# Optimization experiments

Hardware: AMD Instinct MI355X
Metric: run time of the kernel (lower is better)

The kernel has to match this reference:

```python
import jax, jax.numpy as jnp
import numpy as np

N_NODES = 100000

def gcn_conv(x, W, b, src, dst, n):
    # PyG GCNConv: add self-loops, symmetric normalization, scatter-add aggregation.
    xw = x @ W  # [N, out]
    loop = jnp.arange(n, dtype=src.dtype)
    s = jnp.concatenate([src, loop])
    d = jnp.concatenate([dst, loop])
    deg = jax.ops.segment_sum(jnp.ones_like(d, dtype=xw.dtype), d, num_segments=n)
    inv_sqrt = jnp.where(deg > 0, jax.lax.rsqrt(jnp.maximum(deg, 1.0)), 0.0)
    norm = inv_sqrt[s] * inv_sqrt[d]  # [E+N]
    msg = xw[s] * norm[:, None]       # gather + scale
    out = jax.ops.segment_sum(msg, d, num_segments=n)  # scatter-add
    return out + b

def setup_inputs() -> dict:
    key = jax.random.key(0)
    k = jax.random.split(key, 6)
    x = jax.random.normal(k[0], (N_NODES, 128), dtype=jnp.float32)
    edge_index = jax.random.randint(k[1], (2, 3200000), 0, N_NODES, dtype=jnp.int64 if jax.config.jax_enable_x64 else jnp.int32)
    edge_label_index = jax.random.randint(k[2], (2, 200000), 0, N_NODES, dtype=edge_index.dtype)
    W1 = jax.random.normal(k[3], (128, 32), dtype=jnp.float32) * (1.0 / np.sqrt(128))
    b1 = jnp.zeros((32,), dtype=jnp.float32)
    W2 = jax.random.normal(k[4], (32, 16), dtype=jnp.float32) * (1.0 / np.sqrt(32))
    b2 = jnp.zeros((16,), dtype=jnp.float32)
    return {"x": x, "edge_index": edge_index, "edge_label_index": edge_label_index,
            "W1": W1, "b1": b1, "W2": W2, "b2": b2}

def reference(x, edge_index, edge_label_index, W1, b1, W2, b2):
    src, dst = edge_index[0], edge_index[1]
    n = x.shape[0]
    # encode (eval mode: dropout is identity)
    h = gcn_conv(x, W1, b1, src, dst, n)
    h = jax.nn.relu(h)
    z = gcn_conv(h, W2, b2, src, dst, n)
    # decode: dot product over candidate edges
    logits = jnp.sum(z[edge_label_index[0]] * z[edge_label_index[1]], axis=-1)
    return logits
```

## Files before the change

### kernel.cpp

```cpp
#include <hip/hip_runtime.h>
#include <hip/hip_fp16.h>


#define NPB 512
#define NBMAX 256
#define A3_CHUNK 4096

__global__ __launch_bounds__(256) void k_a1(const int* __restrict__ dst,
                                            int* __restrict__ bcnt, int E, int NB) {
    __shared__ int lb[NBMAX];
    int t = threadIdx.x;
    for (int i = t; i < NB; i += 256) lb[i] = 0;
    __syncthreads();
    for (int e = blockIdx.x * 256 + t; e < E; e += gridDim.x * 256)
        atomicAdd(&lb[dst[e] >> 9], 1);
    __syncthreads();
    for (int i = t; i < NB; i += 256) {
        int c = lb[i];
        if (c) atomicAdd(&bcnt[i], c);
    }
}

__global__ __launch_bounds__(256) void k_scanb(const int* __restrict__ bcnt,
                                               int* __restrict__ bbase,
                                               int* __restrict__ bcursor,
                                               int* __restrict__ pbase, int NB) {
    __shared__ int sh[256];
    int t = threadIdx.x;
    int i0 = t * 4;
    int v[4], p[4];
#pragma unroll
    for (int j = 0; j < 4; ++j) {
        v[j] = (i0 + j < NB) ? bcnt[i0 + j] : 0;
        p[j] = ((v[j] + 3) & ~3) + 3 * NPB;
    }
    sh[t] = v[0] + v[1] + v[2] + v[3];
    __syncthreads();
    for (int off = 1; off < 256; off <<= 1) {
        int add = (t >= off) ? sh[t - off] : 0;
        __syncthreads();
        sh[t] += add;
        __syncthreads();
    }
    int run = (t > 0) ? sh[t - 1] : 0;
    int total = sh[255];
#pragma unroll
    for (int j = 0; j < 4; ++j) {
        if (i0 + j < NB) { bbase[i0 + j] = run; bcursor[i0 + j] = run; }
        run += v[j];
    }
    if (t == 255) bbase[NB] = total;
    __syncthreads();
    sh[t] = p[0] + p[1] + p[2] + p[3];
    __syncthreads();
    for (int off = 1; off < 256; off <<= 1) {
        int add = (t >= off) ? sh[t - off] : 0;
        __syncthreads();
        sh[t] += add;
        __syncthreads();
    }
    int run2 = (t > 0) ? sh[t - 1] : 0;
#pragma unroll
    for (int j = 0; j < 4; ++j) {
        if (i0 + j < NB) pbase[i0 + j] = run2;
        run2 += p[j];
    }
}

__global__ __launch_bounds__(256) void k_a3(const int* __restrict__ src,
                                            const int* __restrict__ dst,
                                            int* __restrict__ bcursor,
                                            unsigned* __restrict__ eb, int E, int NB) {
    __shared__ int lhist[NBMAX];
    __shared__ int lbase[NBMAX];
    int t = threadIdx.x;
    int e0 = blockIdx.x * A3_CHUNK;
    int e1 = min(e0 + A3_CHUNK, E);
    for (int i = t; i < NB; i += 256) lhist[i] = 0;
    __syncthreads();
    for (int e = e0 + t; e < e1; e += 256)
        atomicAdd(&lhist[dst[e] >> 9], 1);
    __syncthreads();
    for (int i = t; i < NB; i += 256) {
        int c = lhist[i];
        lbase[i] = c ? atomicAdd(&bcursor[i], c) : 0;
        lhist[i] = 0;
    }
    __syncthreads();
    for (int e = e0 + t; e < e1; e += 256) {
        int s = src[e], d = dst[e];
        int b = d >> 9;
        int r = atomicAdd(&lhist[b], 1);
        eb[lbase[b] + r] = ((unsigned)s << 9) | (unsigned)(d & 511);
    }
}

__global__ __launch_bounds__(256) void k_csr(const int* __restrict__ bbase,
                                             const int* __restrict__ pbase,
                                             const unsigned* __restrict__ eb,
                                             int* __restrict__ col,
                                             int* __restrict__ rpbeg,
                                             int* __restrict__ rpcnt,
                                             float* __restrict__ inv,
                                             int n, int NB) {
    __shared__ int cnt[4][NPB];
    __shared__ int cur[4][NPB];
    __shared__ int sh[256];
    int t = threadIdx.x, b = blockIdx.x;
    int wv = t >> 6;
    int nbase = b * NPB;
    int beg = bbase[b], end = bbase[b + 1];
    int pb = pbase[b];
    for (int i = t; i < 4 * NPB; i += 256) ((int*)cnt)[i] = 0;
    __syncthreads();
    for (int i = beg + t; i < end; i += 256) atomicAdd(&cnt[wv][eb[i] & 511u], 1);
    __syncthreads();
    int l0 = 2 * t, l1 = 2 * t + 1;
    int c0 = cnt[0][l0] + cnt[1][l0] + cnt[2][l0] + cnt[3][l0];
    int c1 = cnt[0][l1] + cnt[1][l1] + cnt[2][l1] + cnt[3][l1];
    int pc0 = (c0 + 3) & ~3, pc1 = (c1 + 3) & ~3;
    sh[t] = pc0 + pc1;
    __syncthreads();
    for (int off = 1; off < 256; off <<= 1) {
        int v = (t >= off) ? sh[t - off] : 0;
        __syncthreads();
        sh[t] += v;
        __syncthreads();
    }
    int base0 = pb + sh[t] - (pc0 + pc1);
    int base1 = base0 + pc0;
    int run = base0;
#pragma unroll
    for (int r = 0; r < 4; ++r) { cur[r][l0] = run; run += cnt[r][l0]; }
    run = base1;
#pragma unroll
    for (int r = 0; r < 4; ++r) { cur[r][l1] = run; run += cnt[r][l1]; }
    int node0 = nbase + l0, node1 = nbase + l1;
    if (node0 < n) {
        rpbeg[node0] = base0;
        rpcnt[node0] = pc0;
        inv[node0] = rsqrtf((float)(c0 + 1));
        for (int j = c0; j < pc0; ++j) col[base0 + j] = n;
    }
    if (node1 < n) {
        rpbeg[node1] = base1;
        rpcnt[node1] = pc1;
        inv[node1] = rsqrtf((float)(c1 + 1));
        for (int j = c1; j < pc1; ++j) col[base1 + j] = n;
    }
    __syncthreads();
    for (int i = beg + t; i < end; i += 256) {
        unsigned p = eb[i];
        int pos = atomicAdd(&cur[wv][p & 511u], 1);
        col[pos] = (int)(p >> 9);
    }
}

__global__ __launch_bounds__(256) void k_xw(const float* __restrict__ x,
                                            const float* __restrict__ W1,
                                            const float* __restrict__ inv,
                                            uint2* __restrict__ X,
                                            unsigned* __restrict__ hws0, int n) {
    __shared__ float xsh[128 * 128];
    __shared__ float W1s[128 * 32];
    int t = threadIdx.x;
    int base = blockIdx.x * 128;
#pragma unroll
    for (int i = 0; i < 16; ++i) W1s[i * 256 + t] = W1[i * 256 + t];
    {
        int nl = t >> 1, kh = (t & 1) * 64;
        int node = base + nl;
        if (node < n) {
            const float4* xr = (const float4*)(x + (size_t)node * 128 + kh);
#pragma unroll
            for (int kk = 0; kk < 16; ++kk) {
                float4 v = xr[kk];
                int k = kh + kk * 4;
                xsh[(k + 0) * 128 + nl] = v.x;
                xsh[(k + 1) * 128 + nl] = v.y;
                xsh[(k + 2) * 128 + nl] = v.z;
                xsh[(k + 3) * 128 + nl] = v.w;
            }
        } else {
#pragma unroll
            for (int kk = 0; kk < 64; ++kk) xsh[(kh + kk) * 128 + nl] = 0.0f;
        }
    }
    if (blockIdx.x == 0) {
        if (t < 8) X[(size_t)n * 8 + t] = make_uint2(0u, 0u);
        else if (t < 16) hws0[(size_t)n * 8 + (t - 8)] = 0u;
    }
    __syncthreads();
    int tc = t & 7, tr = t >> 3;
    float acc[4][4] = {};
#pragma unroll 8
    for (int k = 0; k < 128; ++k) {
        float4 xv = *(const float4*)&xsh[k * 128 + 4 * tr];
        float4 wv = *(const float4*)&W1s[k * 32 + 4 * tc];
        acc[0][0] += xv.x * wv.x; acc[0][1] += xv.x * wv.y; acc[0][2] += xv.x * wv.z; acc[0][3] += xv.x * wv.w;
        acc[1][0] += xv.y * wv.x; acc[1][1] += xv.y * wv.y; acc[1][2] += xv.y * wv.z; acc[1][3] += xv.y * wv.w;
        acc[2][0] += xv.z * wv.x; acc[2][1] += xv.z * wv.y; acc[2][2] += xv.z * wv.z; acc[2][3] += xv.z * wv.w;
        acc[3][0] += xv.w * wv.x; acc[3][1] += xv.w * wv.y; acc[3][2] += xv.w * wv.z; acc[3][3] += xv.w * wv.w;
    }
#pragma unroll
    for (int i = 0; i < 4; ++i) {
        int node = base + 4 * tr + i;
        if (node < n) {
            float iw = inv[node];
            __half2 p0 = __floats2half2_rn(acc[i][0] * iw, acc[i][1] * iw);
            __half2 p1 = __floats2half2_rn(acc[i][2] * iw, acc[i][3] * iw);
            uint2 u;
            u.x = *(unsigned*)&p0;
            u.y = *(unsigned*)&p1;
            X[(size_t)node * 8 + tc] = u;
        }
    }
}

__device__ __forceinline__ void add4h(float* a, uint2 v) {
    union { uint2 u; __half h[4]; } cv;
    cv.u = v;
#pragma unroll
    for (int j = 0; j < 4; ++j) a[j] = fmaf(__half2float(cv.h[j]), 1.0f, a[j]);
}

__device__ __forceinline__ void add2h(float* a, unsigned v) {
    union { unsigned u; __half h[2]; } cv;
    cv.u = v;
    a[0] = fmaf(__half2float(cv.h[0]), 1.0f, a[0]);
    a[1] = fmaf(__half2float(cv.h[1]), 1.0f, a[1]);
}

__global__ __launch_bounds__(256) void k_agg1(const int* __restrict__ rpbeg,
                                              const int* __restrict__ rpcnt,
                                              const int* __restrict__ col,
                                              const uint2* __restrict__ X2,
                                              const float* __restrict__ inv,
                                              const float* __restrict__ b1,
                                              const float* __restrict__ W2,
                                              __half2* __restrict__ hws, int n) {
    __shared__ float W2s[512];
    int t = threadIdx.x;
    W2s[t] = W2[t];
    W2s[256 + t] = W2[256 + t];
    __syncthreads();
    int w = (blockIdx.x * 256 + t) >> 3;
    if (w >= n) return;
    int q = t & 7;
    int grpbase = (t & 63) & 56;
    float bb[4];
#pragma unroll
    for (int j = 0; j < 4; ++j) bb[j] = b1[4 * q + j];
    int beg = rpbeg[w], endp = beg + rpcnt[w];
    float a[4] = {};
    add4h(a, X2[(size_t)w * 8 + q]);
    for (int i = beg; i < endp; i += 4) {
        int4 c4 = *(const int4*)(col + i);
        uint2 v0 = X2[(size_t)c4.x * 8 + q];
        uint2 v1 = X2[(size_t)c4.y * 8 + q];
        uint2 v2 = X2[(size_t)c4.z * 8 + q];
        uint2 v3 = X2[(size_t)c4.w * 8 + q];
        add4h(a, v0);
        add4h(a, v1);
        add4h(a, v2);
        add4h(a, v3);
    }
    float iw = inv[w];
    float h[4];
#pragma unroll
    for (int j = 0; j < 4; ++j) h[j] = fmaxf(iw * a[j] + bb[j], 0.0f);
    float s0 = 0.0f, s1 = 0.0f;
#pragma unroll
    for (int qq = 0; qq < 8; ++qq) {
#pragma unroll
        for (int j = 0; j < 4; ++j) {
            float hv = __shfl(h[j], grpbase + qq);
            float2 wv = *(const float2*)&W2s[(4 * qq + j) * 16 + 2 * q];
            s0 = fmaf(hv, wv.x, s0);
            s1 = fmaf(hv, wv.y, s1);
        }
    }
    hws[(size_t)w * 8 + q] = __floats2half2_rn(s0 * iw, s1 * iw);
}

__global__ __launch_bounds__(256) void k_agg2(const int* __restrict__ rpbeg,
                                              const int* __restrict__ rpcnt,
                                              const int* __restrict__ col,
                                              const unsigned* __restrict__ H,
                                              const float* __restrict__ inv,
                                              const float* __restrict__ b2,
                                              unsigned* __restrict__ z, int n) {
    int t = threadIdx.x;
    int w = (blockIdx.x * 256 + t) >> 3;
    if (w >= n) return;
    int q = t & 7;
    float bb0 = b2[2 * q], bb1 = b2[2 * q + 1];
    int beg = rpbeg[w], endp = beg + rpcnt[w];
    float a[2] = {};
    add2h(a, H[(size_t)w * 8 + q]);
    for (int i = beg; i < endp; i += 4) {
        int4 c4 = *(const int4*)(col + i);
        unsigned v0 = H[(size_t)c4.x * 8 + q];
        unsigned v1 = H[(size_t)c4.y * 8 + q];
        unsigned v2 = H[(size_t)c4.z * 8 + q];
        unsigned v3 = H[(size_t)c4.w * 8 + q];
        add2h(a, v0);
        add2h(a, v1);
        add2h(a, v2);
        add2h(a, v3);
    }
    float iw = inv[w];
    __half2 r = __floats2half2_rn(iw * a[0] + bb0, iw * a[1] + bb1);
    z[(size_t)w * 8 + q] = *(unsigned*)&r;
}

__device__ __forceinline__ float dot8h(uint4 u, uint4 v, float s) {
    const __half2* pu = (const __half2*)&u;
    const __half2* pv = (const __half2*)&v;
#pragma unroll
    for (int i = 0; i < 4; ++i) {
#if __has_builtin(__builtin_amdgcn_fdot2)
        s = __builtin_amdgcn_fdot2(pu[i], pv[i], s, false);
#else
        float2 a = __half22float2(pu[i]);
        float2 b = __half22float2(pv[i]);
        s += a.x * b.x + a.y * b.y;
#endif
    }
    return s;
}

__global__ void k_decode(const int* __restrict__ eli, const uint4* __restrict__ z4,
                         float* __restrict__ out, int L) {
    int e = blockIdx.x * blockDim.x + threadIdx.x;
    if (e >= L) return;
    int a = eli[e], b = eli[L + e];
    uint4 ua0 = z4[(size_t)a * 2], ua1 = z4[(size_t)a * 2 + 1];
    uint4 ub0 = z4[(size_t)b * 2], ub1 = z4[(size_t)b * 2 + 1];
    out[e] = dot8h(ua1, ub1, dot8h(ua0, ub0, 0.0f));
}

extern "C" void kernel_launch(void* const* d_in, const int* in_sizes, int n_in,
                              void* d_out, int out_size, void* d_ws, size_t ws_size,
                              hipStream_t stream) {
    const float* x   = (const float*)d_in[0];
    const int*   ei  = (const int*)d_in[1];
    const int*   eli = (const int*)d_in[2];
    const float* W1  = (const float*)d_in[3];
    const float* b1  = (const float*)d_in[4];
    const float* W2  = (const float*)d_in[5];
    const float* b2  = (const float*)d_in[6];
    float* out = (float*)d_out;

    int n = in_sizes[0] / 128;
    int E = in_sizes[1] / 2;
    int L = in_sizes[2] / 2;
    const int* src = ei;
    const int* dst = ei + E;
    int NB = (n + NPB - 1) / NPB;

    uint2* X       = (uint2*)d_ws;
    unsigned* hws  = (unsigned*)(X + (size_t)(n + 1) * 8);
    unsigned* z    = hws + (size_t)(n + 1) * 8;
    float* inv     = (float*)(z + (size_t)n * 8);
    int* rpbeg     = (int*)(inv + n);
    int* rpcnt     = rpbeg + n;
    unsigned* eb   = (unsigned*)(rpcnt + n);
    int* col       = (int*)(eb + E);
    int* bcnt      = col + E + 1600 * NB;
    int* bbase     = bcnt + NB;
    int* pbase     = bbase + NB + 1;
    int* bcursor   = pbase + NB + 1;

    hipMemsetAsync(bcnt, 0, NB * sizeof(int), stream);
    k_a1<<<512, 256, 0, stream>>>(dst, bcnt, E, NB);
    k_scanb<<<1, 256, 0, stream>>>(bcnt, bbase, bcursor, pbase, NB);
    k_a3<<<(E + A3_CHUNK - 1) / A3_CHUNK, 256, 0, stream>>>(src, dst, bcursor, eb, E, NB);
    k_csr<<<NB, 256, 0, stream>>>(bbase, pbase, eb, col, rpbeg, rpcnt, inv, n, NB);
    k_xw<<<(n + 127) / 128, 256, 0, stream>>>(x, W1, inv, X, hws, n);
    k_agg1<<<((size_t)n * 8 + 255) / 256, 256, 0, stream>>>(rpbeg, rpcnt, col, X, inv, b1, W2, (__half2*)hws, n);
    k_agg2<<<((size_t)n * 8 + 255) / 256, 256, 0, stream>>>(rpbeg, rpcnt, col, hws, inv, b2, z, n);
    k_decode<<<(L + 255) / 256, 256, 0, stream>>>(eli, (const uint4*)z, out, L);
}
```

Baseline: 313.4 us.

## Replace atomic bucket partition with deterministic per-chunk histogram, scan and LDS-staged scatter

```diff
diff --git a/kernel.cpp b/kernel.cpp
--- a/kernel.cpp
+++ b/kernel.cpp
@@ -4,99 +4,99 @@
 
 #define NPB 512
 #define NBMAX 256
-#define A3_CHUNK 4096
-
-__global__ __launch_bounds__(256) void k_a1(const int* __restrict__ dst,
-                                            int* __restrict__ bcnt, int E, int NB) {
-    __shared__ int lb[NBMAX];
-    int t = threadIdx.x;
-    for (int i = t; i < NB; i += 256) lb[i] = 0;
-    __syncthreads();
-    for (int e = blockIdx.x * 256 + t; e < E; e += gridDim.x * 256)
-        atomicAdd(&lb[dst[e] >> 9], 1);
-    __syncthreads();
-    for (int i = t; i < NB; i += 256) {
-        int c = lb[i];
-        if (c) atomicAdd(&bcnt[i], c);
-    }
-}
-
-__global__ __launch_bounds__(256) void k_scanb(const int* __restrict__ bcnt,
-                                               int* __restrict__ bbase,
-                                               int* __restrict__ bcursor,
-                                               int* __restrict__ pbase, int NB) {
+#define CHUNK 4096
+#define CAP 18432
+#define PCAP (CAP + 3 * NPB)
+
+__global__ __launch_bounds__(256) void k_hist(const int* __restrict__ dst,
+                                              int* __restrict__ cnt, int E, int NB) {
+    __shared__ int lh[NBMAX];
+    int t = threadIdx.x, c = blockIdx.x;
+    int e0 = c * CHUNK, e1 = min(e0 + CHUNK, E);
+    for (int i = t; i < NB; i += 256) lh[i] = 0;
+    __syncthreads();
+    for (int e = e0 + t; e < e1; e += 256) atomicAdd(&lh[dst[e] >> 9], 1);
+    __syncthreads();
+    for (int i = t; i < NB; i += 256) cnt[c * NB + i] = lh[i];
+}
+
+__global__ __launch_bounds__(256) void k_bscan(const int* __restrict__ cnt,
+                                               int* __restrict__ rbase,
+                                               int* __restrict__ bcnt,
+                                               int NC, int NB) {
     __shared__ int sh[256];
-    int t = threadIdx.x;
-    int i0 = t * 4;
-    int v[4], p[4];
+    int t = threadIdx.x, b = blockIdx.x;
+    int v[4];
+    int part = 0;
 #pragma unroll
     for (int j = 0; j < 4; ++j) {
-        v[j] = (i0 + j < NB) ? bcnt[i0 + j] : 0;
-        p[j] = ((v[j] + 3) & ~3) + 3 * NPB;
-    }
-    sh[t] = v[0] + v[1] + v[2] + v[3];
+        int c = t * 4 + j;
+        v[j] = (c < NC) ? cnt[c * NB + b] : 0;
+        part += v[j];
+    }
+    sh[t] = part;
     __syncthreads();
     for (int off = 1; off < 256; off <<= 1) {
-        int add = (t >= off) ? sh[t - off] : 0;
-        __syncthreads();
-        sh[t] += add;
-        __syncthreads();
-    }
-    int run = (t > 0) ? sh[t - 1] : 0;
-    int total = sh[255];
+        int a = (t >= off) ? sh[t - off] : 0;
+        __syncthreads();
+        sh[t] += a;
+        __syncthreads();
+    }
+    int run = b * CAP + sh[t] - part;
 #pragma unroll
     for (int j = 0; j < 4; ++j) {
-        if (i0 + j < NB) { bbase[i0 + j] = run; bcursor[i0 + j] = run; }
+        int c = t * 4 + j;
+        if (c < NC) rbase[c * NB + b] = run;
         run += v[j];
     }
-    if (t == 255) bbase[NB] = total;
-    __syncthreads();
-    sh[t] = p[0] + p[1] + p[2] + p[3];
+    if (t == 255) bcnt[b] = sh[255];
+}
+
+__global__ __launch_bounds__(256) void k_scatter(const int* __restrict__ src,
+                                                 const int* __restrict__ dst,
+                                                 const int* __restrict__ cnt,
+                                                 const int* __restrict__ rbase,
+                                                 unsigned* __restrict__ eb,
+                                                 int E, int NB) {
+    __shared__ unsigned buf[CHUNK];
+    __shared__ int lcnt[NBMAX];
+    __shared__ int lbase[NBMAX];
+    __shared__ int gbase[NBMAX];
+    __shared__ int lrank[NBMAX];
+    __shared__ int sh[256];
+    int t = threadIdx.x, c = blockIdx.x;
+    int e0 = c * CHUNK, e1 = min(e0 + CHUNK, E);
+    int myc = (t < NB) ? cnt[c * NB + t] : 0;
+    if (t < NB) {
+        lcnt[t] = myc;
+        gbase[t] = rbase[c * NB + t];
+        lrank[t] = 0;
+    }
+    sh[t] = myc;
     __syncthreads();
     for (int off = 1; off < 256; off <<= 1) {
-        int add = (t >= off) ? sh[t - off] : 0;
-        __syncthreads();
-        sh[t] += add;
-        __syncthreads();
-    }
-    int run2 = (t > 0) ? sh[t - 1] : 0;
-#pragma unroll
-    for (int j = 0; j < 4; ++j) {
-        if (i0 + j < NB) pbase[i0 + j] = run2;
-        run2 += p[j];
-    }
-}
-
-__global__ __launch_bounds__(256) void k_a3(const int* __restrict__ src,
-                                            const int* __restrict__ dst,
-                                            int* __restrict__ bcursor,
-                                            unsigned* __restrict__ eb, int E, int NB) {
-    __shared__ int lhist[NBMAX];
-    __shared__ int lbase[NBMAX];
-    int t = threadIdx.x;
-    int e0 = blockIdx.x * A3_CHUNK;
-    int e1 = min(e0 + A3_CHUNK, E);
-    for (int i = t; i < NB; i += 256) lhist[i] = 0;
-    __syncthreads();
-    for (int e = e0 + t; e < e1; e += 256)
-        atomicAdd(&lhist[dst[e] >> 9], 1);
-    __syncthreads();
-    for (int i = t; i < NB; i += 256) {
-        int c = lhist[i];
-        lbase[i] = c ? atomicAdd(&bcursor[i], c) : 0;
-        lhist[i] = 0;
-    }
+        int a = (t >= off) ? sh[t - off] : 0;
+        __syncthreads();
+        sh[t] += a;
+        __syncthreads();
+    }
+    if (t < NB) lbase[t] = sh[t] - myc;
     __syncthreads();
     for (int e = e0 + t; e < e1; e += 256) {
         int s = src[e], d = dst[e];
         int b = d >> 9;
-        int r = atomicAdd(&lhist[b], 1);
-        eb[lbase[b] + r] = ((unsigned)s << 9) | (unsigned)(d & 511);
-    }
-}
-
-__global__ __launch_bounds__(256) void k_csr(const int* __restrict__ bbase,
-                                             const int* __restrict__ pbase,
+        int r = atomicAdd(&lrank[b], 1);
+        buf[lbase[b] + r] = ((unsigned)s << 9) | (unsigned)(d & 511);
+    }
+    __syncthreads();
+    int wv = t >> 6, lane = t & 63;
+    for (int b = wv; b < NB; b += 4) {
+        int base = lbase[b], gb = gbase[b], len = lcnt[b];
+        for (int i = lane; i < len; i += 64) eb[gb + i] = buf[base + i];
+    }
+}
+
+__global__ __launch_bounds__(256) void k_csr(const int* __restrict__ bcnt,
                                              const unsigned* __restrict__ eb,
                                              int* __restrict__ col,
                                              int* __restrict__ rpbeg,
@@ -109,8 +109,8 @@
     int t = threadIdx.x, b = blockIdx.x;
     int wv = t >> 6;
     int nbase = b * NPB;
-    int beg = bbase[b], end = bbase[b + 1];
-    int pb = pbase[b];
+    int beg = b * CAP, end = beg + bcnt[b];
+    int pb = b * PCAP;
     for (int i = t; i < 4 * NPB; i += 256) ((int*)cnt)[i] = 0;
     __syncthreads();
     for (int i = beg + t; i < end; i += 256) atomicAdd(&cnt[wv][eb[i] & 511u], 1);
@@ -358,6 +358,7 @@
     const int* src = ei;
     const int* dst = ei + E;
     int NB = (n + NPB - 1) / NPB;
+    int NC = (E + CHUNK - 1) / CHUNK;
 
     uint2* X       = (uint2*)d_ws;
     unsigned* hws  = (unsigned*)(X + (size_t)(n + 1) * 8);
@@ -366,17 +367,15 @@
     int* rpbeg     = (int*)(inv + n);
     int* rpcnt     = rpbeg + n;
     unsigned* eb   = (unsigned*)(rpcnt + n);
-    int* col       = (int*)(eb + E);
-    int* bcnt      = col + E + 1600 * NB;
-    int* bbase     = bcnt + NB;
-    int* pbase     = bbase + NB + 1;
-    int* bcursor   = pbase + NB + 1;
-
-    hipMemsetAsync(bcnt, 0, NB * sizeof(int), stream);
-    k_a1<<<512, 256, 0, stream>>>(dst, bcnt, E, NB);
-    k_scanb<<<1, 256, 0, stream>>>(bcnt, bbase, bcursor, pbase, NB);
-    k_a3<<<(E + A3_CHUNK - 1) / A3_CHUNK, 256, 0, stream>>>(src, dst, bcursor, eb, E, NB);
-    k_csr<<<NB, 256, 0, stream>>>(bbase, pbase, eb, col, rpbeg, rpcnt, inv, n, NB);
+    int* col       = (int*)(eb + (size_t)NB * CAP);
+    int* cnt       = col + (size_t)NB * PCAP;
+    int* rbase     = cnt + (size_t)NC * NB;
+    int* bcnt      = rbase + (size_t)NC * NB;
+
+    k_hist<<<NC, 256, 0, stream>>>(dst, cnt, E, NB);
+    k_bscan<<<NB, 256, 0, stream>>>(cnt, rbase, bcnt, NC, NB);
+    k_scatter<<<NC, 256, 0, stream>>>(src, dst, cnt, rbase, eb, E, NB);
+    k_csr<<<NB, 256, 0, stream>>>(bcnt, eb, col, rpbeg, rpcnt, inv, n, NB);
     k_xw<<<(n + 127) / 128, 256, 0, stream>>>(x, W1, inv, X, hws, n);
     k_agg1<<<((size_t)n * 8 + 255) / 256, 256, 0, stream>>>(rpbeg, rpcnt, col, X, inv, b1, W2, (__half2*)hws, n);
     k_agg2<<<((size_t)n * 8 + 255) / 256, 256, 0, stream>>>(rpbeg, rpcnt, col, hws, inv, b2, z, n);
```

Result: faster. 262.8 us (-16.2%).
